# Performance work log

Hardware: AMD Instinct MI355X
Metric: run time of the kernel (lower is better)

The kernel has to match this reference:

```python
import jax, jax.numpy as jnp
import numpy as np

B = 8
INPUT_DIM = 6670   # upper-triangle of 116x116 FC matrix (AAL atlas)
N = 116
FD = 16
HEADS = (8, 4, 1)
DIMS = (128, 256, 512)
NC = 2
THR = 0.5
EPS = 1e-5


def _glorot(key, shape):
    s = (2.0 / (shape[0] + shape[-1])) ** 0.5
    return jax.random.normal(key, shape, dtype=jnp.float32) * s


def setup_inputs() -> dict:
    key = jax.random.key(0)
    ks = iter(jax.random.split(key, 64))
    inp = {}
    inp['x'] = jax.random.normal(next(ks), (B, INPUT_DIM), dtype=jnp.float32)
    # DynamicGraphBuilder params
    inp['W_gb'] = _glorot(next(ks), (INPUT_DIM, N * N))
    inp['b_gb'] = jnp.zeros((N * N,), jnp.float32)
    inp['fe_W1'] = _glorot(next(ks), (2, 8)); inp['fe_b1'] = jnp.zeros((8,), jnp.float32)
    inp['fe_W2'] = _glorot(next(ks), (8, FD)); inp['fe_b2'] = jnp.zeros((FD,), jnp.float32)
    inp['ln_g'] = jnp.ones((FD,), jnp.float32); inp['ln_b'] = jnp.zeros((FD,), jnp.float32)
    # GATv2 layers
    prev = FD
    for l, (d, h) in enumerate(zip(DIMS, HEADS)):
        inp['Wl%d' % l] = _glorot(next(ks), (prev, h * d))
        inp['bl%d' % l] = jnp.zeros((h * d,), jnp.float32)
        inp['Wr%d' % l] = _glorot(next(ks), (prev, h * d))
        inp['br%d' % l] = jnp.zeros((h * d,), jnp.float32)
        inp['att%d' % l] = _glorot(next(ks), (h, d))
        inp['bias%d' % l] = jnp.zeros((h * d,), jnp.float32)
        prev = h * d
    # classifier
    inp['Wc1'] = _glorot(next(ks), (prev, 256)); inp['bc1'] = jnp.zeros((256,), jnp.float32)
    inp['bn_g'] = jnp.ones((256,), jnp.float32); inp['bn_b'] = jnp.zeros((256,), jnp.float32)
    inp['Wc2'] = _glorot(next(ks), (256, NC)); inp['bc2'] = jnp.zeros((NC,), jnp.float32)
    return inp


def _gatv2(hx, mask_st, Wl, bl, Wr, br, att, bias, heads, out_dim, self_loops):
    # mask_st[b, src, tgt] True if edge src->tgt exists (PyG flow source_to_target)
    Bn, Nn, _ = hx.shape
    if self_loops:  # PyG remove_self_loops + add_self_loops => diag forced present
        mask_st = mask_st | jnp.eye(Nn, dtype=bool)
    xl = (hx @ Wl + bl).reshape(Bn, Nn, heads, out_dim)  # source transform
    xr = (hx @ Wr + br).reshape(Bn, Nn, heads, out_dim)  # target transform
    # pairwise: axis1 = target i, axis2 = source j  -> [B, i, j, h, o]
    z = jax.nn.leaky_relu(xr[:, :, None] + xl[:, None, :], 0.2)
    e = jnp.einsum('bijho,ho->bhij', z, att)  # [B, h, tgt, src]
    m = jnp.swapaxes(mask_st, 1, 2)[:, None]  # [B, 1, tgt, src]
    em = jnp.where(m, e, -1e30)
    emax = jnp.max(em, axis=-1, keepdims=True)
    p = jnp.exp(em - emax) * m  # zero for masked / empty rows
    alpha = p / jnp.maximum(p.sum(-1, keepdims=True), 1e-16)
    out = jnp.einsum('bhij,bjho->biho', alpha, xl).reshape(Bn, Nn, heads * out_dim)
    return out + bias


def _forward(x, W_gb, b_gb, fe_W1, fe_b1, fe_W2, fe_b2, ln_g, ln_b,
             Wl0, bl0, Wr0, br0, att0, bias0,
             Wl1, bl1, Wr1, br1, att1, bias1,
             Wl2, bl2, Wr2, br2, att2, bias2,
             Wc1, bc1, bn_g, bn_b, Wc2, bc2):
    Bn = x.shape[0]
    adj = jax.nn.sigmoid(x @ W_gb + b_gb).reshape(Bn, N, N)
    mask = adj > THR                      # edge (row -> col) exists
    adj_t = jnp.where(mask, adj, 0.0)     # thresholded adjacency
    mu = adj_t.mean(-1)                   # torch mean(dim=1) on [N,N]
    std = jnp.sqrt(jnp.sum((adj_t - mu[..., None]) ** 2, -1) / (N - 1))  # unbiased
    stats = jnp.stack([mu, std], -1)      # [B, N, 2]
    hfe = jax.nn.gelu(stats @ fe_W1 + fe_b1, approximate=False) @ fe_W2 + fe_b2
    lm = hfe.mean(-1, keepdims=True)
    lv = jnp.mean((hfe - lm) ** 2, -1, keepdims=True)
    h = (hfe - lm) / jnp.sqrt(lv + EPS) * ln_g + ln_b  # [B, N, FD]
    convs = [
        (Wl0, bl0, Wr0, br0, att0, bias0, HEADS[0], DIMS[0], False),
        (Wl1, bl1, Wr1, br1, att1, bias1, HEADS[1], DIMS[1], True),
        (Wl2, bl2, Wr2, br2, att2, bias2, HEADS[2], DIMS[2], True),
    ]
    for (Wl, bl, Wr, br, att, bias, hh, dd, sl) in convs:
        h = jax.nn.gelu(_gatv2(h, mask, Wl, bl, Wr, br, att, bias, hh, dd, sl), approximate=False)
    pooled = h.mean(1)                    # global_mean_pool per graph
    c = pooled @ Wc1 + bc1
    c = c / jnp.sqrt(1.0 + EPS) * bn_g + bn_b  # BatchNorm1d eval (running mean 0, var 1)
    c = jax.nn.gelu(c, approximate=False)
    return c @ Wc2 + bc2


def reference(x, W_gb, b_gb, fe_W1, fe_b1, fe_W2, fe_b2, ln_g, ln_b,
              Wl0, bl0, Wr0, br0, att0, bias0,
              Wl1, bl1, Wr1, br1, att1, bias1,
              Wl2, bl2, Wr2, br2, att2, bias2,
              Wc1, bc1, bn_g, bn_b, Wc2, bc2):
    return _forward(x, W_gb, b_gb, fe_W1, fe_b1, fe_W2, fe_b2, ln_g, ln_b,
                    Wl0, bl0, Wr0, br0, att0, bias0,
                    Wl1, bl1, Wr1, br1, att1, bias1,
                    Wl2, bl2, Wr2, br2, att2, bias2,
                    Wc1, bc1, bn_g, bn_b, Wc2, bc2)
```

## Files before the change

### kernel.cpp

```cpp
#include <hip/hip_runtime.h>
#include <math.h>


#define NB 8
#define NN 116
#define NN2 (NN*NN)
#define KIN 6670
#define FD 16
#define KCHUNK 32
#define KSTEP 209

__device__ __forceinline__ float gelu_f(float x) {
  return 0.5f * x * (1.0f + erff(x * 0.70710678118654752f));
}
__device__ __forceinline__ float lrelu(float x) {
  return fmaxf(x, 0.2f * x);
}

__global__ void k_transpose_x(const float* __restrict__ x, float* __restrict__ xT) {
  int idx = blockIdx.x * 256 + threadIdx.x;
  if (idx >= NB * KIN) return;
  int b = idx / KIN, k = idx % KIN;
  xT[k * NB + b] = x[idx];
}

__global__ __launch_bounds__(256) void k_gemm_big(
    const float* __restrict__ xT, const float* __restrict__ Wg,
    float* __restrict__ partial) {
  int c0 = (blockIdx.x * 256 + threadIdx.x) * 4;
  if (c0 >= NN2) return;
  int chunk = blockIdx.y;
  int k0 = chunk * KSTEP;
  int k1 = min(k0 + KSTEP, KIN);
  float acc[NB][4];
#pragma unroll
  for (int b = 0; b < NB; b++)
#pragma unroll
    for (int c = 0; c < 4; c++) acc[b][c] = 0.f;
#pragma unroll 2
  for (int k = k0; k < k1; ++k) {
    const float4 xa = *(const float4*)(xT + k * NB);
    const float4 xb = *(const float4*)(xT + k * NB + 4);
    float4 wv = *(const float4*)(Wg + (size_t)k * NN2 + c0);
    float w[4] = {wv.x, wv.y, wv.z, wv.w};
    float xs[NB] = {xa.x, xa.y, xa.z, xa.w, xb.x, xb.y, xb.z, xb.w};
#pragma unroll
    for (int b = 0; b < NB; b++)
#pragma unroll
      for (int c = 0; c < 4; c++)
        acc[b][c] = fmaf(xs[b], w[c], acc[b][c]);
  }
#pragma unroll
  for (int b = 0; b < NB; b++)
#pragma unroll
    for (int c = 0; c < 4; c++)
      partial[((size_t)chunk * NB + b) * NN2 + c0 + c] = acc[b][c];
}

__global__ void k_reduce_sigmoid(const float* __restrict__ partial,
                                 const float* __restrict__ bgb,
                                 float* __restrict__ adj) {
  int t = blockIdx.x * 256 + threadIdx.x;
  if (t >= NB * NN2) return;
  int b = t / NN2, rc = t % NN2;
  float s = bgb[rc];
#pragma unroll 8
  for (int ch = 0; ch < KCHUNK; ch++)
    s += partial[((size_t)ch * NB + b) * NN2 + rc];
  adj[t] = 1.0f / (1.0f + expf(-s));
}

__global__ void k_stats(const float* __restrict__ adj,
                        const float* __restrict__ feW1, const float* __restrict__ feb1,
                        const float* __restrict__ feW2, const float* __restrict__ feb2,
                        const float* __restrict__ lng, const float* __restrict__ lnb,
                        float* __restrict__ h0) {
  int b = blockIdx.x;
  int r = threadIdx.x;
  if (r >= NN) return;
  const float* row = adj + (size_t)(b * NN + r) * NN;
  float sum = 0.f;
  for (int c = 0; c < NN; c++) { float a = row[c]; sum += (a > 0.5f) ? a : 0.f; }
  float mu = sum / (float)NN;
  float ss = 0.f;
  for (int c = 0; c < NN; c++) {
    float a = row[c]; float m = (a > 0.5f) ? a : 0.f;
    float d = m - mu; ss += d * d;
  }
  float sd = sqrtf(ss / (float)(NN - 1));
  float hid[8];
#pragma unroll
  for (int a = 0; a < 8; a++) {
    float z = mu * feW1[a] + sd * feW1[8 + a] + feb1[a];
    hid[a] = gelu_f(z);
  }
  float hf[FD];
  float lm = 0.f;
#pragma unroll
  for (int o = 0; o < FD; o++) {
    float z = feb2[o];
#pragma unroll
    for (int a = 0; a < 8; a++) z += hid[a] * feW2[a * FD + o];
    hf[o] = z; lm += z;
  }
  lm /= (float)FD;
  float lv = 0.f;
#pragma unroll
  for (int o = 0; o < FD; o++) { float d = hf[o] - lm; lv += d * d; }
  lv /= (float)FD;
  float inv = 1.0f / sqrtf(lv + 1e-5f);
#pragma unroll
  for (int o = 0; o < FD; o++)
    h0[(size_t)(b * NN + r) * FD + o] = (hf[o] - lm) * inv * lng[o] + lnb[o];
}

#define GM 64
#define GN 64
#define GK 32
__global__ __launch_bounds__(256) void k_gemm_dual(
    const float* __restrict__ A,
    const float* __restrict__ W0, const float* __restrict__ b0,
    const float* __restrict__ W1, const float* __restrict__ b1,
    float* __restrict__ C0, float* __restrict__ C1,
    int M, int K, int N) {
  int nc = blockIdx.x * GN;
  const float* W    = (nc < N) ? W0 : W1;
  const float* bias = (nc < N) ? b0 : b1;
  float*       C    = (nc < N) ? C0 : C1;
  int n0 = (nc < N) ? nc : nc - N;
  int m0 = blockIdx.y * GM;

  __shared__ float a_s[GK][GM];
  __shared__ float b_s[GK][GN + 4];
  int t = threadIdx.x;
  int tx = t & 15, ty = t >> 4;
  float acc[4][4];
#pragma unroll
  for (int i = 0; i < 4; i++)
#pragma unroll
    for (int j = 0; j < 4; j++) acc[i][j] = 0.f;

  for (int kt = 0; kt < K; kt += GK) {
    {
      int m = t & 63, k8 = (t >> 6) * 8;
      int gm = m0 + m;
      float va[8];
      if (gm < M && (kt + k8 + 8) <= K) {
        float4 v0 = *(const float4*)(A + (size_t)gm * K + kt + k8);
        float4 v1 = *(const float4*)(A + (size_t)gm * K + kt + k8 + 4);
        va[0]=v0.x; va[1]=v0.y; va[2]=v0.z; va[3]=v0.w;
        va[4]=v1.x; va[5]=v1.y; va[6]=v1.z; va[7]=v1.w;
      } else {
#pragma unroll
        for (int e = 0; e < 8; e++) {
          int gk = kt + k8 + e;
          va[e] = (gm < M && gk < K) ? A[(size_t)gm * K + gk] : 0.f;
        }
      }
#pragma unroll
      for (int e = 0; e < 8; e++) a_s[k8 + e][m] = va[e];
    }
    {
      int k = t >> 3, n8 = (t & 7) * 8;
      int gk = kt + k;
      float4 w0 = make_float4(0.f,0.f,0.f,0.f), w1 = w0;
      if (gk < K) {
        const float* wp = W + (size_t)gk * N + n0 + n8;
        w0 = *(const float4*)(wp);
        w1 = *(const float4*)(wp + 4);
      }
      b_s[k][n8 + 0] = w0.x; b_s[k][n8 + 1] = w0.y;
      b_s[k][n8 + 2] = w0.z; b_s[k][n8 + 3] = w0.w;
      b_s[k][n8 + 4] = w1.x; b_s[k][n8 + 5] = w1.y;
      b_s[k][n8 + 6] = w1.z; b_s[k][n8 + 7] = w1.w;
    }
    __syncthreads();
#pragma unroll
    for (int kk = 0; kk < GK; kk++) {
      float4 av = *(const float4*)(&a_s[kk][ty << 2]);
      float4 bv = *(const float4*)(&b_s[kk][tx << 2]);
      float am[4] = {av.x, av.y, av.z, av.w};
      float bn_[4] = {bv.x, bv.y, bv.z, bv.w};
#pragma unroll
      for (int i = 0; i < 4; i++)
#pragma unroll
        for (int j = 0; j < 4; j++)
          acc[i][j] = fmaf(am[i], bn_[j], acc[i][j]);
    }
    __syncthreads();
  }
#pragma unroll
  for (int i = 0; i < 4; i++) {
    int m = m0 + (ty << 2) + i;
    if (m >= M) break;
#pragma unroll
    for (int j = 0; j < 4; j++) {
      int n = n0 + (tx << 2) + j;
      C[(size_t)m * N + n] = acc[i][j] + bias[n];
    }
  }
}

template<int HH_, int DD_>
__global__ __launch_bounds__(256) void k_attn_aggr(
    const float* __restrict__ xl, const float* __restrict__ xr,
    const float* __restrict__ adj, const float* __restrict__ att,
    const float* __restrict__ bias, float* __restrict__ hout, int selfloop) {
  constexpr int HD = HH_ * DD_;
  __shared__ float xr_lds[HD];
  __shared__ float att_lds[HD];
  __shared__ float e_lds[HH_][128];
  __shared__ float maskf[128];
  int i = blockIdx.x, b = blockIdx.y;
  int t = threadIdx.x;

  for (int idx = t; idx < HD; idx += 256) {
    xr_lds[idx]  = xr[(size_t)(b * NN + i) * HD + idx];
    att_lds[idx] = att[idx];
  }
  if (t < 128) {
    bool mj = (t < NN) && ((adj[(size_t)(b * NN + t) * NN + i] > 0.5f) ||
                           (selfloop && (t == i)));
    maskf[t] = mj ? 1.f : 0.f;
  }
  __syncthreads();

  int half = t >> 7;
  int j = t & 127;
  bool valid = (j < NN);
  const float* xlj = xl + (size_t)(b * NN + (valid ? j : 0)) * HD;
  if (HH_ >= 2) {
    constexpr int HHH = HH_ / 2;
#pragma unroll
    for (int hh = 0; hh < HHH; hh++) {
      int h = half * HHH + hh;
      int base = h * DD_;
      float acc = 0.f;
      for (int o = 0; o < DD_; o += 4) {
        float4 v = *(const float4*)(xlj + base + o);
        acc = fmaf(att_lds[base + o + 0], lrelu(xr_lds[base + o + 0] + v.x), acc);
        acc = fmaf(att_lds[base + o + 1], lrelu(xr_lds[base + o + 1] + v.y), acc);
        acc = fmaf(att_lds[base + o + 2], lrelu(xr_lds[base + o + 2] + v.z), acc);
        acc = fmaf(att_lds[base + o + 3], lrelu(xr_lds[base + o + 3] + v.w), acc);
      }
      if (valid) e_lds[h][j] = acc;
    }
    __syncthreads();
  } else {
    constexpr int DH = DD_ / 2;
    int base = half * DH;
    float acc = 0.f;
    for (int o = 0; o < DH; o += 4) {
      float4 v = *(const float4*)(xlj + base + o);
      acc = fmaf(att_lds[base + o + 0], lrelu(xr_lds[base + o + 0] + v.x), acc);
      acc = fmaf(att_lds[base + o + 1], lrelu(xr_lds[base + o + 1] + v.y), acc);
      acc = fmaf(att_lds[base + o + 2], lrelu(xr_lds[base + o + 2] + v.z), acc);
      acc = fmaf(att_lds[base + o + 3], lrelu(xr_lds[base + o + 3] + v.w), acc);
    }
    if (half == 0 && valid) e_lds[0][j] = acc;
    __syncthreads();
    if (half == 1 && valid) e_lds[0][j] += acc;
    __syncthreads();
  }

  {
    int w = t >> 6, lane = t & 63;
#pragma unroll
    for (int hh = 0; hh < (HH_ + 3) / 4; hh++) {
      int h = w + hh * 4;
      if (h < HH_) {
        float mk0 = maskf[lane], mk1 = maskf[lane + 64];
        float e0 = e_lds[h][lane], e1 = e_lds[h][lane + 64];
        float v = fmaxf(mk0 != 0.f ? e0 : -3.0e38f,
                        mk1 != 0.f ? e1 : -3.0e38f);
#pragma unroll
        for (int o = 32; o; o >>= 1) v = fmaxf(v, __shfl_xor(v, o, 64));
        float p0 = (mk0 != 0.f) ? expf(e0 - v) : 0.f;
        float p1 = (mk1 != 0.f) ? expf(e1 - v) : 0.f;
        float s = p0 + p1;
#pragma unroll
        for (int o = 32; o; o >>= 1) s += __shfl_xor(s, o, 64);
        float inv = 1.0f / fmaxf(s, 1e-16f);
        e_lds[h][lane]      = p0 * inv;
        e_lds[h][lane + 64] = p1 * inv;
      }
    }
  }
  __syncthreads();

  for (int c = t; c < HD; c += 256) {
    int h = c / DD_;
    const float* xp = xl + (size_t)b * NN * HD + c;
    const float* arow = e_lds[h];
    float acc = 0.f;
#pragma unroll 4
    for (int jj = 0; jj < NN; jj++)
      acc = fmaf(arow[jj], xp[(size_t)jj * HD], acc);
    hout[(size_t)(b * NN + i) * HD + c] = gelu_f(acc + bias[c]);
  }
}

__global__ __launch_bounds__(256) void k_classifier(
    const float* __restrict__ hfin,
    const float* __restrict__ Wc1, const float* __restrict__ bc1,
    const float* __restrict__ bng, const float* __restrict__ bnb,
    const float* __restrict__ Wc2, const float* __restrict__ bc2,
    float* __restrict__ out) {
  __shared__ float pooled[512];
  __shared__ float cls[256];
  int b = blockIdx.x;
  int t = threadIdx.x;
#pragma unroll
  for (int r = 0; r < 2; r++) {
    int c = t + (r << 8);
    float s = 0.f;
    for (int i = 0; i < NN; i++) s += hfin[(size_t)(b * NN + i) * 512 + c];
    pooled[c] = s / (float)NN;
  }
  __syncthreads();
  {
    int n = t;
    float acc = bc1[n];
    for (int k = 0; k < 512; k++)
      acc = fmaf(pooled[k], Wc1[k * 256 + n], acc);
    float c = acc * (1.0f / sqrtf(1.0f + 1e-5f)) * bng[n] + bnb[n];
    cls[n] = gelu_f(c);
  }
  __syncthreads();
  if (t < 128) {
    int jj = t >> 6, lane = t & 63;
    float s = 0.f;
#pragma unroll
    for (int w = 0; w < 4; w++) {
      int k = lane + (w << 6);
      s += cls[k] * Wc2[k * 2 + jj];
    }
#pragma unroll
    for (int o = 32; o; o >>= 1) s += __shfl_xor(s, o, 64);
    if (lane == 0) out[b * 2 + jj] = s + bc2[jj];
  }
}

extern "C" void kernel_launch(void* const* d_in, const int* in_sizes, int n_in,
                              void* d_out, int out_size, void* d_ws, size_t ws_size,
                              hipStream_t stream) {
  const float* x    = (const float*)d_in[0];
  const float* Wgb  = (const float*)d_in[1];
  const float* bgb  = (const float*)d_in[2];
  const float* feW1 = (const float*)d_in[3];
  const float* feb1 = (const float*)d_in[4];
  const float* feW2 = (const float*)d_in[5];
  const float* feb2 = (const float*)d_in[6];
  const float* lng  = (const float*)d_in[7];
  const float* lnb  = (const float*)d_in[8];
  const float* Wl[3]   = {(const float*)d_in[9],  (const float*)d_in[15], (const float*)d_in[21]};
  const float* bl[3]   = {(const float*)d_in[10], (const float*)d_in[16], (const float*)d_in[22]};
  const float* Wr[3]   = {(const float*)d_in[11], (const float*)d_in[17], (const float*)d_in[23]};
  const float* br[3]   = {(const float*)d_in[12], (const float*)d_in[18], (const float*)d_in[24]};
  const float* att[3]  = {(const float*)d_in[13], (const float*)d_in[19], (const float*)d_in[25]};
  const float* bias[3] = {(const float*)d_in[14], (const float*)d_in[20], (const float*)d_in[26]};
  const float* Wc1 = (const float*)d_in[27];
  const float* bc1 = (const float*)d_in[28];
  const float* bng = (const float*)d_in[29];
  const float* bnb = (const float*)d_in[30];
  const float* Wc2 = (const float*)d_in[31];
  const float* bc2 = (const float*)d_in[32];

  float* ws = (float*)d_ws;
  float* xT  = ws;
  float* adj = ws + 53376;
  float* scratch = ws + 161024;
  float* partial = scratch;
  float* hA      = scratch;
  float* hB      = hA + 950272;
  float* xlbuf   = hB + 950272;
  float* xrbuf   = xlbuf + 950272;

  k_transpose_x<<<dim3((NB * KIN + 255) / 256), 256, 0, stream>>>(x, xT);
  k_gemm_big<<<dim3(14, KCHUNK), 256, 0, stream>>>(xT, Wgb, partial);
  k_reduce_sigmoid<<<dim3((NB * NN2 + 255) / 256), 256, 0, stream>>>(partial, bgb, adj);
  k_stats<<<dim3(NB), 128, 0, stream>>>(adj, feW1, feb1, feW2, feb2, lng, lnb, hA);

  dim3 ab(NN, NB);
  k_gemm_dual<<<dim3(2 * 1024 / GN, 15), 256, 0, stream>>>(
      hA, Wl[0], bl[0], Wr[0], br[0], xlbuf, xrbuf, 928, 16, 1024);
  k_attn_aggr<8, 128><<<ab, 256, 0, stream>>>(xlbuf, xrbuf, adj, att[0], bias[0], hB, 0);
  k_gemm_dual<<<dim3(2 * 1024 / GN, 15), 256, 0, stream>>>(
      hB, Wl[1], bl[1], Wr[1], br[1], xlbuf, xrbuf, 928, 1024, 1024);
  k_attn_aggr<4, 256><<<ab, 256, 0, stream>>>(xlbuf, xrbuf, adj, att[1], bias[1], hA, 1);
  k_gemm_dual<<<dim3(2 * 512 / GN, 15), 256, 0, stream>>>(
      hA, Wl[2], bl[2], Wr[2], br[2], xlbuf, xrbuf, 928, 1024, 512);
  k_attn_aggr<1, 512><<<ab, 256, 0, stream>>>(xlbuf, xrbuf, adj, att[2], bias[2], hB, 1);

  k_classifier<<<dim3(NB), 256, 0, stream>>>(hB, Wc1, bc1, bng, bnb, Wc2, bc2,
                                             (float*)d_out);
}
```

Baseline: 974.7 us.

## Process four target nodes per attention block and deepen big-GEMM K split

The GATv2 attention/aggregation kernel now handles four target nodes per block. Each xl row and each att vector loaded from memory is reused across four targets when computing scores, and each xl column read is reused across four output rows during aggregation. This cuts redundant global traffic on xl but leaves only 29x8 blocks, which may underfill the GPU. Separately, the large graph-builder GEMM moves to 64 K-chunks with a deeper unroll to raise parallelism for the weight stream, at the cost of twice as much partial-sum storage and reduction work.

New measurement: 907.3 us. -6.9%, faster.

```diff
diff --git a/kernel.cpp b/kernel.cpp
--- a/kernel.cpp
+++ b/kernel.cpp
@@ -7,8 +7,8 @@
 #define NN2 (NN*NN)
 #define KIN 6670
 #define FD 16
-#define KCHUNK 32
-#define KSTEP 209
+#define KCHUNK 64
+#define KSTEP 105
 
 __device__ __forceinline__ float gelu_f(float x) {
   return 0.5f * x * (1.0f + erff(x * 0.70710678118654752f));
@@ -37,7 +37,7 @@
   for (int b = 0; b < NB; b++)
 #pragma unroll
     for (int c = 0; c < 4; c++) acc[b][c] = 0.f;
-#pragma unroll 2
+#pragma unroll 4
   for (int k = k0; k < k1; ++k) {
     const float4 xa = *(const float4*)(xT + k * NB);
     const float4 xb = *(const float4*)(xT + k * NB + 4);
@@ -207,21 +207,27 @@
     const float* __restrict__ adj, const float* __restrict__ att,
     const float* __restrict__ bias, float* __restrict__ hout, int selfloop) {
   constexpr int HD = HH_ * DD_;
-  __shared__ float xr_lds[HD];
+  __shared__ float xr_lds[4][HD];
   __shared__ float att_lds[HD];
-  __shared__ float e_lds[HH_][128];
-  __shared__ float maskf[128];
-  int i = blockIdx.x, b = blockIdx.y;
+  __shared__ __align__(16) float e_lds[HH_][128][4];
+  __shared__ float maskf[4][128];
+  int i0 = blockIdx.x * 4, b = blockIdx.y;
   int t = threadIdx.x;
 
   for (int idx = t; idx < HD; idx += 256) {
-    xr_lds[idx]  = xr[(size_t)(b * NN + i) * HD + idx];
     att_lds[idx] = att[idx];
+#pragma unroll
+    for (int ti = 0; ti < 4; ti++)
+      xr_lds[ti][idx] = xr[(size_t)(b * NN + i0 + ti) * HD + idx];
   }
   if (t < 128) {
-    bool mj = (t < NN) && ((adj[(size_t)(b * NN + t) * NN + i] > 0.5f) ||
-                           (selfloop && (t == i)));
-    maskf[t] = mj ? 1.f : 0.f;
+#pragma unroll
+    for (int ti = 0; ti < 4; ti++) {
+      int i = i0 + ti;
+      bool mj = (t < NN) && ((adj[(size_t)(b * NN + t) * NN + i] > 0.5f) ||
+                             (selfloop && (t == i)));
+      maskf[ti][t] = mj ? 1.f : 0.f;
+    }
   }
   __syncthreads();
 
@@ -229,74 +235,105 @@
   int j = t & 127;
   bool valid = (j < NN);
   const float* xlj = xl + (size_t)(b * NN + (valid ? j : 0)) * HD;
-  if (HH_ >= 2) {
+  if constexpr (HH_ >= 2) {
     constexpr int HHH = HH_ / 2;
 #pragma unroll
     for (int hh = 0; hh < HHH; hh++) {
       int h = half * HHH + hh;
       int base = h * DD_;
-      float acc = 0.f;
+      float acc[4] = {0.f, 0.f, 0.f, 0.f};
       for (int o = 0; o < DD_; o += 4) {
-        float4 v = *(const float4*)(xlj + base + o);
-        acc = fmaf(att_lds[base + o + 0], lrelu(xr_lds[base + o + 0] + v.x), acc);
-        acc = fmaf(att_lds[base + o + 1], lrelu(xr_lds[base + o + 1] + v.y), acc);
-        acc = fmaf(att_lds[base + o + 2], lrelu(xr_lds[base + o + 2] + v.z), acc);
-        acc = fmaf(att_lds[base + o + 3], lrelu(xr_lds[base + o + 3] + v.w), acc);
+        float4 v  = *(const float4*)(xlj + base + o);
+        float4 af = *(const float4*)(att_lds + base + o);
+#pragma unroll
+        for (int ti = 0; ti < 4; ti++) {
+          float4 r = *(const float4*)(&xr_lds[ti][base + o]);
+          float a = acc[ti];
+          a = fmaf(af.x, lrelu(r.x + v.x), a);
+          a = fmaf(af.y, lrelu(r.y + v.y), a);
+          a = fmaf(af.z, lrelu(r.z + v.z), a);
+          a = fmaf(af.w, lrelu(r.w + v.w), a);
+          acc[ti] = a;
+        }
       }
-      if (valid) e_lds[h][j] = acc;
+      if (valid)
+        *(float4*)(&e_lds[h][j][0]) = make_float4(acc[0], acc[1], acc[2], acc[3]);
     }
     __syncthreads();
   } else {
     constexpr int DH = DD_ / 2;
     int base = half * DH;
-    float acc = 0.f;
+    float acc[4] = {0.f, 0.f, 0.f, 0.f};
     for (int o = 0; o < DH; o += 4) {
-      float4 v = *(const float4*)(xlj + base + o);
-      acc = fmaf(att_lds[base + o + 0], lrelu(xr_lds[base + o + 0] + v.x), acc);
-      acc = fmaf(att_lds[base + o + 1], lrelu(xr_lds[base + o + 1] + v.y), acc);
-      acc = fmaf(att_lds[base + o + 2], lrelu(xr_lds[base + o + 2] + v.z), acc);
-      acc = fmaf(att_lds[base + o + 3], lrelu(xr_lds[base + o + 3] + v.w), acc);
-    }
-    if (half == 0 && valid) e_lds[0][j] = acc;
+      float4 v  = *(const float4*)(xlj + base + o);
+      float4 af = *(const float4*)(att_lds + base + o);
+#pragma unroll
+      for (int ti = 0; ti < 4; ti++) {
+        float4 r = *(const float4*)(&xr_lds[ti][base + o]);
+        float a = acc[ti];
+        a = fmaf(af.x, lrelu(r.x + v.x), a);
+        a = fmaf(af.y, lrelu(r.y + v.y), a);
+        a = fmaf(af.z, lrelu(r.z + v.z), a);
+        a = fmaf(af.w, lrelu(r.w + v.w), a);
+        acc[ti] = a;
+      }
+    }
+    if (half == 0 && valid)
+      *(float4*)(&e_lds[0][j][0]) = make_float4(acc[0], acc[1], acc[2], acc[3]);
     __syncthreads();
-    if (half == 1 && valid) e_lds[0][j] += acc;
+    if (half == 1 && valid) {
+      float4 p = *(const float4*)(&e_lds[0][j][0]);
+      p.x += acc[0]; p.y += acc[1]; p.z += acc[2]; p.w += acc[3];
+      *(float4*)(&e_lds[0][j][0]) = p;
+    }
     __syncthreads();
   }
 
   {
     int w = t >> 6, lane = t & 63;
-#pragma unroll
-    for (int hh = 0; hh < (HH_ + 3) / 4; hh++) {
-      int h = w + hh * 4;
-      if (h < HH_) {
-        float mk0 = maskf[lane], mk1 = maskf[lane + 64];
-        float e0 = e_lds[h][lane], e1 = e_lds[h][lane + 64];
-        float v = fmaxf(mk0 != 0.f ? e0 : -3.0e38f,
-                        mk1 != 0.f ? e1 : -3.0e38f);
-#pragma unroll
-        for (int o = 32; o; o >>= 1) v = fmaxf(v, __shfl_xor(v, o, 64));
-        float p0 = (mk0 != 0.f) ? expf(e0 - v) : 0.f;
-        float p1 = (mk1 != 0.f) ? expf(e1 - v) : 0.f;
-        float s = p0 + p1;
-#pragma unroll
-        for (int o = 32; o; o >>= 1) s += __shfl_xor(s, o, 64);
-        float inv = 1.0f / fmaxf(s, 1e-16f);
-        e_lds[h][lane]      = p0 * inv;
-        e_lds[h][lane + 64] = p1 * inv;
-      }
+    for (int fh = w; fh < 4 * HH_; fh += 4) {
+      int ti = fh / HH_, h = fh - ti * HH_;
+      float mk0 = maskf[ti][lane], mk1 = maskf[ti][lane + 64];
+      float e0 = e_lds[h][lane][ti], e1 = e_lds[h][lane + 64][ti];
+      float v = fmaxf(mk0 != 0.f ? e0 : -3.0e38f,
+                      mk1 != 0.f ? e1 : -3.0e38f);
+#pragma unroll
+      for (int o = 32; o; o >>= 1) v = fmaxf(v, __shfl_xor(v, o, 64));
+      float p0 = (mk0 != 0.f) ? expf(e0 - v) : 0.f;
+      float p1 = (mk1 != 0.f) ? expf(e1 - v) : 0.f;
+      float s = p0 + p1;
+#pragma unroll
+      for (int o = 32; o; o >>= 1) s += __shfl_xor(s, o, 64);
+      float inv = 1.0f / fmaxf(s, 1e-16f);
+      e_lds[h][lane][ti]      = p0 * inv;
+      e_lds[h][lane + 64][ti] = p1 * inv;
     }
   }
   __syncthreads();
 
-  for (int c = t; c < HD; c += 256) {
+  constexpr int CITER = HD / 256;
+  const float* xb = xl + (size_t)b * NN * HD;
+  float* hb = hout + (size_t)(b * NN + i0) * HD;
+#pragma unroll
+  for (int it = 0; it < CITER; it++) {
+    int c = t + (it << 8);
     int h = c / DD_;
-    const float* xp = xl + (size_t)b * NN * HD + c;
-    const float* arow = e_lds[h];
-    float acc = 0.f;
+    const float* xp = xb + c;
+    float a0 = 0.f, a1 = 0.f, a2 = 0.f, a3 = 0.f;
 #pragma unroll 4
-    for (int jj = 0; jj < NN; jj++)
-      acc = fmaf(arow[jj], xp[(size_t)jj * HD], acc);
-    hout[(size_t)(b * NN + i) * HD + c] = gelu_f(acc + bias[c]);
+    for (int jj = 0; jj < NN; jj++) {
+      float xv = xp[(size_t)jj * HD];
+      float4 al = *(const float4*)(&e_lds[h][jj][0]);
+      a0 = fmaf(al.x, xv, a0);
+      a1 = fmaf(al.y, xv, a1);
+      a2 = fmaf(al.z, xv, a2);
+      a3 = fmaf(al.w, xv, a3);
+    }
+    float bv = bias[c];
+    hb[c]          = gelu_f(a0 + bv);
+    hb[HD + c]     = gelu_f(a1 + bv);
+    hb[2 * HD + c] = gelu_f(a2 + bv);
+    hb[3 * HD + c] = gelu_f(a3 + bv);
   }
 }
 
@@ -381,7 +418,7 @@
   k_reduce_sigmoid<<<dim3((NB * NN2 + 255) / 256), 256, 0, stream>>>(partial, bgb, adj);
   k_stats<<<dim3(NB), 128, 0, stream>>>(adj, feW1, feb1, feW2, feb2, lng, lnb, hA);
 
-  dim3 ab(NN, NB);
+  dim3 ab(NN / 4, NB);
   k_gemm_dual<<<dim3(2 * 1024 / GN, 15), 256, 0, stream>>>(
       hA, Wl[0], bl[0], Wr[0], br[0], xlbuf, xrbuf, 928, 16, 1024);
   k_attn_aggr<8, 128><<<ab, 256, 0, stream>>>(xlbuf, xrbuf, adj, att[0], bias[0], hB, 0);
```
